# Kernel tuning notes

Measured on AMD Instinct MI355X. Metric: run time of the kernel, lower is better.

The kernel has to match this reference:

```python
import jax, jax.numpy as jnp
import numpy as np

N_NODES = 200_000
N_EDGES = 6_400_000
N_GRAPHS = 512


def _graph_conv(x, src, dst, W_rel, b_rel, W_root, n_nodes):
    # PyG GraphConv (aggr='add'): lin_rel(sum_{j->i} x_j) + lin_root(x_i)
    agg = jax.ops.segment_sum(x[src], dst, num_segments=n_nodes)  # [N, in]
    return agg @ W_rel.T + b_rel + x @ W_root.T


def setup_inputs() -> dict:
    key = jax.random.key(0)
    ks = jax.random.split(key, 12)
    x = jax.random.normal(ks[0], (N_NODES, 3), dtype=jnp.float32)
    edge_index = jax.random.randint(ks[1], (2, N_EDGES), 0, N_NODES, dtype=jnp.int64)
    batch = jnp.sort(jax.random.randint(ks[2], (N_NODES,), 0, N_GRAPHS, dtype=jnp.int64))

    def xavier(k, shape):
        fan_out, fan_in = shape
        lim = np.sqrt(6.0 / (fan_in + fan_out)).astype(np.float32)
        return jax.random.uniform(k, shape, jnp.float32, -lim, lim)

    return {
        "x": x, "edge_index": edge_index, "batch": batch,
        "W1_rel": xavier(ks[3], (32, 3)),  "b1": jnp.zeros((32,), jnp.float32), "W1_root": xavier(ks[4], (32, 3)),
        "W2_rel": xavier(ks[5], (16, 32)), "b2": jnp.zeros((16,), jnp.float32), "W2_root": xavier(ks[6], (16, 32)),
        "W3_rel": xavier(ks[7], (8, 16)),  "b3": jnp.zeros((8,), jnp.float32),  "W3_root": xavier(ks[8], (8, 16)),
        "W_lin": xavier(ks[9], (1, 8)),    "b_lin": jnp.zeros((1,), jnp.float32),
    }


def reference(x, edge_index, batch,
              W1_rel, b1, W1_root,
              W2_rel, b2, W2_root,
              W3_rel, b3, W3_root,
              W_lin, b_lin):
    src, dst = edge_index[0], edge_index[1]
    h = jax.nn.relu(_graph_conv(x, src, dst, W1_rel, b1, W1_root, N_NODES))
    h = jax.nn.relu(_graph_conv(h, src, dst, W2_rel, b2, W2_root, N_NODES))
    h = jax.nn.relu(_graph_conv(h, src, dst, W3_rel, b3, W3_root, N_NODES))
    pooled = jax.ops.segment_max(h, batch, num_segments=N_GRAPHS)  # [G, 8]
    out = pooled @ W_lin.T + b_lin  # [G, 1]
    return out[:, 0]
```

## Files before the change

### kernel.cpp

```cpp
#include <hip/hip_runtime.h>
#include <hip/hip_fp16.h>

#define N_NODES 200000
#define N_EDGES 6400000
#define N_GRAPHS 512
#define HALFN 100000

#define NB1 196
#define CB 1024
#define NSB 16
#define NFB (NB1 * NSB)
#define CHUNK 4096
#define NCH 1563
#define NGRP 25
#define CPG 63
#define SCAP 3072
#define NBLK32 (N_NODES / 32)

typedef float vf4 __attribute__((ext_vector_type(4)));
typedef float vf2 __attribute__((ext_vector_type(2)));
typedef unsigned vu2 __attribute__((ext_vector_type(2)));

__device__ __forceinline__ unsigned ntload_u(const unsigned* p) {
  return __builtin_nontemporal_load(p);
}
__device__ __forceinline__ int ntload_i(const int* p) { return __builtin_nontemporal_load(p); }
__device__ __forceinline__ float ntload_f(const float* p) {
  return __builtin_nontemporal_load(p);
}
__device__ __forceinline__ void ntstore_u(unsigned* p, unsigned v) {
  __builtin_nontemporal_store(v, p);
}

__global__ __launch_bounds__(256) void count_kernel(const int* __restrict__ dst,
                                                    unsigned short* __restrict__ H) {
  __shared__ unsigned hist[4][NB1];
  int t = threadIdx.x, w = t >> 6;
  for (int i = t; i < 4 * NB1; i += 256) ((unsigned*)hist)[i] = 0;
  __syncthreads();
  int c = blockIdx.x;
  long e0 = (long)c * CHUNK;
  long rem = (long)N_EDGES - e0;
  int n = rem > CHUNK ? CHUNK : (int)rem;
  for (int i = t; i < n; i += 256) atomicAdd(&hist[w][dst[e0 + i] >> 10], 1u);
  __syncthreads();
  for (int b = t; b < NB1; b += 256)
    H[(size_t)c * NB1 + b] =
        (unsigned short)(hist[0][b] + hist[1][b] + hist[2][b] + hist[3][b]);
}

__global__ __launch_bounds__(256) void scan_bins1_kernel(unsigned short* __restrict__ H,
                                                         unsigned* __restrict__ P) {
  int b = blockIdx.x * 256 + threadIdx.x;
  int g = blockIdx.y;
  if (b >= NB1) return;
  int c0 = g * CPG, c1 = min(NCH, (g + 1) * CPG);
  unsigned run = 0;
  for (int c = c0; c < c1; c++) {
    unsigned t = H[(size_t)c * NB1 + b];
    H[(size_t)c * NB1 + b] = (unsigned short)run;
    run += t;
  }
  P[(size_t)g * NB1 + b] = run;
}

__global__ __launch_bounds__(256) void scan_bins2_kernel(unsigned* __restrict__ P,
                                                         unsigned* __restrict__ bucketTotal) {
  int b = blockIdx.x * 256 + threadIdx.x;
  if (b >= NB1) return;
  unsigned run = 0;
  for (int g = 0; g < NGRP; g++) {
    unsigned t = P[(size_t)g * NB1 + b];
    P[(size_t)g * NB1 + b] = run;
    run += t;
  }
  bucketTotal[b] = run;
}

__global__ __launch_bounds__(256) void scan_total_kernel(const unsigned* __restrict__ bucketTotal,
                                                         unsigned* __restrict__ bucketStart) {
  __shared__ unsigned partial[256];
  int t = threadIdx.x;
  unsigned v = (t < NB1) ? bucketTotal[t] : 0u;
  partial[t] = v;
  __syncthreads();
  for (int off = 1; off < 256; off <<= 1) {
    unsigned add = (t >= off) ? partial[t - off] : 0u;
    __syncthreads();
    partial[t] += add;
    __syncthreads();
  }
  if (t < NB1) bucketStart[t] = partial[t] - v;
  if (t == 0) bucketStart[NB1] = N_EDGES;
}

__global__ __launch_bounds__(256) void scatterA_kernel(
    const int* __restrict__ src, const int* __restrict__ dst,
    const unsigned short* __restrict__ H, const unsigned* __restrict__ P,
    const unsigned* __restrict__ bucketStart, unsigned* __restrict__ X1) {
  __shared__ unsigned ssort[CHUNK];
  __shared__ unsigned char sbort[CHUNK];
  __shared__ unsigned histw[4][NB1];
  __shared__ unsigned curw[4][NB1];
  __shared__ unsigned gbase[NB1];
  __shared__ unsigned partial[256];
  int t = threadIdx.x, w = t >> 6;
  int c = blockIdx.x;
  int g = c / CPG;
  long e0 = (long)c * CHUNK;
  long rem = (long)N_EDGES - e0;
  int n = rem > CHUNK ? CHUNK : (int)rem;
  for (int i = t; i < 4 * NB1; i += 256) ((unsigned*)histw)[i] = 0;
  __syncthreads();
  for (int i = t; i < n; i += 256) atomicAdd(&histw[w][dst[e0 + i] >> 10], 1u);
  __syncthreads();
  unsigned tot = 0, h0 = 0, h1 = 0, h2 = 0, h3 = 0;
  if (t < NB1) {
    h0 = histw[0][t]; h1 = histw[1][t]; h2 = histw[2][t]; h3 = histw[3][t];
    tot = h0 + h1 + h2 + h3;
  }
  partial[t] = tot;
  __syncthreads();
  for (int off = 1; off < 256; off <<= 1) {
    unsigned add = (t >= off) ? partial[t - off] : 0u;
    __syncthreads();
    partial[t] += add;
    __syncthreads();
  }
  if (t < NB1) {
    unsigned ex = partial[t] - tot;
    unsigned r = ex;
    curw[0][t] = r; r += h0;
    curw[1][t] = r; r += h1;
    curw[2][t] = r; r += h2;
    curw[3][t] = r;
    gbase[t] = bucketStart[t] + P[(size_t)g * NB1 + t] + (unsigned)H[(size_t)c * NB1 + t] - ex;
  }
  __syncthreads();
  for (int i = t; i < n; i += 256) {
    int d = dst[e0 + i], s = src[e0 + i];
    int b = d >> 10;
    unsigned r = atomicAdd(&curw[w][b], 1u);
    ssort[r] = ((unsigned)s << 10) | (unsigned)(d & 1023);
    sbort[r] = (unsigned char)b;
  }
  __syncthreads();
  for (int j = t; j < n; j += 256) X1[gbase[sbort[j]] + j] = ssort[j];
}

__global__ __launch_bounds__(1024) void scatterB_kernel(
    const unsigned* __restrict__ X1, const unsigned* __restrict__ bucketStart,
    unsigned* __restrict__ X2, unsigned* __restrict__ fineStart) {
  __shared__ unsigned histw[16][NSB];
  __shared__ unsigned binstart[NSB + 1];
  __shared__ unsigned cur[NSB];
  int t = threadIdx.x, w = t >> 6, b = blockIdx.x;
  unsigned cs0 = bucketStart[b], cs1 = bucketStart[b + 1];
  int n = (int)(cs1 - cs0);
  if (t < 16 * NSB) ((unsigned*)histw)[t] = 0;
  __syncthreads();
  for (int i = t; i < n; i += 1024)
    atomicAdd(&histw[w][(X1[cs0 + i] >> 6) & 15u], 1u);
  __syncthreads();
  if (t == 0) {
    unsigned run = 0;
    for (int k = 0; k < NSB; k++) {
      binstart[k] = run;
      unsigned tot = 0;
      for (int ww = 0; ww < 16; ww++) tot += histw[ww][k];
      run += tot;
    }
    binstart[NSB] = run;
  }
  __syncthreads();
  if (t < NSB) {
    fineStart[b * NSB + t] = cs0 + binstart[t];
    cur[t] = binstart[t];
  }
  if (b == NB1 - 1 && t == 0) fineStart[NFB] = cs1;
  __syncthreads();
  for (int i = t; i < n; i += 1024) {
    unsigned v = X1[cs0 + i];
    unsigned pos = atomicAdd(&cur[(v >> 6) & 15u], 1u);
    X2[cs0 + pos] = v;
  }
}

__global__ __launch_bounds__(256) void sort2_kernel(const unsigned* __restrict__ X2,
                                                    const unsigned* __restrict__ fineStart,
                                                    unsigned* __restrict__ packedB,
                                                    unsigned* __restrict__ nodeStart,
                                                    unsigned char* __restrict__ deltaSplit) {
  __shared__ unsigned buf[SCAP];
  __shared__ unsigned buf2[SCAP];
  __shared__ unsigned hist[128], base[128], cur[128];
  int t = threadIdx.x, b = blockIdx.x;
  unsigned s0 = fineStart[b], s1 = fineStart[b + 1];
  int n = (int)(s1 - s0);
  if (t < 128) hist[t] = 0;
  for (int i = t; i < n; i += 256) buf[i] = ntload_u(&X2[s0 + i]);
  __syncthreads();
  for (int i = t; i < n; i += 256) {
    unsigned v = buf[i];
    unsigned bin = ((v & 63u) << 1) | ((v >> 10) >= HALFN ? 1u : 0u);
    atomicAdd(&hist[bin], 1u);
  }
  __syncthreads();
  if (t == 0) {
    unsigned run = 0;
    for (int k = 0; k < 128; k++) {
      unsigned v = hist[k];
      base[k] = run;
      cur[k] = run;
      run += v;
    }
  }
  __syncthreads();
  if (t < 64) {
    int gn = b * 64 + t;
    if (gn <= N_NODES) nodeStart[gn] = s0 + base[2 * t];
    if (gn < N_NODES) deltaSplit[gn] = (unsigned char)(base[2 * t + 1] - base[2 * t]);
  }
  for (int i = t; i < n; i += 256) {
    unsigned v = buf[i];
    unsigned bin = ((v & 63u) << 1) | ((v >> 10) >= HALFN ? 1u : 0u);
    unsigned pos = atomicAdd(&cur[bin], 1u);
    buf2[pos] = v >> 10;
  }
  __syncthreads();
  for (int i = t; i < n; i += 256) ntstore_u(&packedB[s0 + i], buf2[i]);
}

__global__ __launch_bounds__(256) void xpad_kernel(const float* __restrict__ x,
                                                   float4* __restrict__ xp) {
  int n = blockIdx.x * 256 + threadIdx.x;
  if (n >= N_NODES) return;
  xp[n] = make_float4(x[3 * n], x[3 * n + 1], x[3 * n + 2], 0.f);
}

__device__ __forceinline__ void half8_unpack(uint4 g, float* f) {
  const __half2* h2 = reinterpret_cast<const __half2*>(&g);
#pragma unroll
  for (int j = 0; j < 4; j++) {
    float2 fj = __half22float2(h2[j]);
    f[2 * j] = fj.x;
    f[2 * j + 1] = fj.y;
  }
}

__global__ __launch_bounds__(256) void layer1a_kernel(
    const unsigned* __restrict__ packed, const unsigned* __restrict__ nodeStart,
    const float4* __restrict__ xp, float* __restrict__ agg) {
  __shared__ float plds[256 * 9];
  int t = threadIdx.x, ln = t >> 3, p = t & 7;
  int node = blockIdx.x * 32 + ln;
  unsigned s1v = ntload_u(&nodeStart[node + 1]);
  float a0 = 0.f, a1 = 0.f, a2 = 0.f;
  for (unsigned base = ntload_u(&nodeStart[node]) + p; base < s1v; base += 32) {
    unsigned i1 = base + 8, i2 = base + 16, i3 = base + 24;
    unsigned e0 = ntload_u(&packed[base]);
    unsigned e1 = ntload_u(&packed[i1]);
    unsigned e2 = ntload_u(&packed[i2]);
    unsigned e3 = ntload_u(&packed[i3]);
    float4 g0 = xp[e0], g1 = xp[e1], g2 = xp[e2], g3 = xp[e3];
    float m1 = (i1 < s1v) ? 1.f : 0.f;
    float m2 = (i2 < s1v) ? 1.f : 0.f;
    float m3 = (i3 < s1v) ? 1.f : 0.f;
    a0 += g0.x + m1 * g1.x + m2 * g2.x + m3 * g3.x;
    a1 += g0.y + m1 * g1.y + m2 * g2.y + m3 * g3.y;
    a2 += g0.z + m1 * g1.z + m2 * g2.z + m3 * g3.z;
  }
  plds[t * 9] = a0; plds[t * 9 + 1] = a1; plds[t * 9 + 2] = a2;
  __syncthreads();
  if (p < 4) {
    int q0 = ln * 72 + p;
    float v = 0.f;
    if (p < 3)
      v = plds[q0] + plds[q0 + 9] + plds[q0 + 18] + plds[q0 + 27] +
          plds[q0 + 36] + plds[q0 + 45] + plds[q0 + 54] + plds[q0 + 63];
    agg[(size_t)node * 4 + p] = v;
  }
}

__global__ __launch_bounds__(256) void layer1b_kernel(
    const float4* __restrict__ xp, const float4* __restrict__ agg,
    const float* __restrict__ W1_rel, const float* __restrict__ b1,
    const float* __restrict__ W1_root,
    const float* __restrict__ W2_rel, const float* __restrict__ W2_root,
    uint4* __restrict__ t2h4, float4* __restrict__ r24) {
  __shared__ float sW1rel[96], sW1root[96], sb1[32], sW2rel[512], sW2root[512];
  for (int i = threadIdx.x; i < 96; i += 256) { sW1rel[i] = W1_rel[i]; sW1root[i] = W1_root[i]; }
  for (int i = threadIdx.x; i < 32; i += 256) sb1[i] = b1[i];
  for (int i = threadIdx.x; i < 512; i += 256) { sW2rel[i] = W2_rel[i]; sW2root[i] = W2_root[i]; }
  __syncthreads();
  int node = blockIdx.x * 256 + threadIdx.x;
  if (node >= N_NODES) return;
  float4 A = agg[node];
  float4 xv = xp[node];
  float h[32];
#pragma unroll
  for (int k = 0; k < 32; k++) {
    float v = sW1rel[3 * k] * A.x + sW1rel[3 * k + 1] * A.y + sW1rel[3 * k + 2] * A.z +
              sW1root[3 * k] * xv.x + sW1root[3 * k + 1] * xv.y + sW1root[3 * k + 2] * xv.z +
              sb1[k];
    h[k] = fmaxf(v, 0.f);
  }
  unsigned tp[8];
#pragma unroll
  for (int j = 0; j < 16; j += 2) {
    float t0 = 0.f, t1 = 0.f;
#pragma unroll
    for (int k = 0; k < 32; k++) {
      t0 += sW2rel[32 * j + k] * h[k];
      t1 += sW2rel[32 * (j + 1) + k] * h[k];
    }
    __half2 pk = __halves2half2(__float2half_rn(t0), __float2half_rn(t1));
    tp[j >> 1] = *(unsigned*)&pk;
  }
  t2h4[(size_t)node * 2] = make_uint4(tp[0], tp[1], tp[2], tp[3]);
  t2h4[(size_t)node * 2 + 1] = make_uint4(tp[4], tp[5], tp[6], tp[7]);
#pragma unroll
  for (int q = 0; q < 4; q++) {
    float rv[4];
#pragma unroll
    for (int jj = 0; jj < 4; jj++) {
      int j = 4 * q + jj;
      float a = 0.f;
#pragma unroll
      for (int k = 0; k < 32; k++) a += sW2root[32 * j + k] * h[k];
      rv[jj] = a;
    }
    r24[(size_t)node * 4 + q] = make_float4(rv[0], rv[1], rv[2], rv[3]);
  }
}

__global__ __launch_bounds__(256) void layer2g_kernel(
    const unsigned* __restrict__ packed, const unsigned* __restrict__ nodeStart,
    const unsigned char* __restrict__ deltaSplit,
    const uint4* __restrict__ t2h4, __half* __restrict__ agg2, int pass) {
  __shared__ float plds[256 * 17];
  int t = threadIdx.x, ln = t >> 3, p = t & 7;
  int node = blockIdx.x * 32 + ln;
  unsigned s0n = ntload_u(&nodeStart[node]);
  unsigned s1n = ntload_u(&nodeStart[node + 1]);
  unsigned split = s0n + (unsigned)deltaSplit[node];
  unsigned lo = pass ? split : s0n;
  unsigned hi = pass ? s1n : split;
  float acc[16];
#pragma unroll
  for (int j = 0; j < 16; j++) acc[j] = 0.f;
  for (unsigned base = lo + p; base < hi; base += 16) {
    unsigned i1 = base + 8;
    unsigned e0 = ntload_u(&packed[base]);
    unsigned e1r = ntload_u(&packed[i1]);
    bool in1 = i1 < hi;
    unsigned e1 = in1 ? e1r : e0;
    uint4 g0a = t2h4[(size_t)e0 * 2], g0b = t2h4[(size_t)e0 * 2 + 1];
    uint4 g1a = t2h4[(size_t)e1 * 2], g1b = t2h4[(size_t)e1 * 2 + 1];
    float f0[16], f1[16];
    half8_unpack(g0a, f0);
    half8_unpack(g0b, f0 + 8);
    half8_unpack(g1a, f1);
    half8_unpack(g1b, f1 + 8);
    float m1 = in1 ? 1.f : 0.f;
#pragma unroll
    for (int j = 0; j < 16; j++) acc[j] += f0[j] + m1 * f1[j];
  }
#pragma unroll
  for (int j = 0; j < 16; j++) plds[t * 17 + j] = acc[j];
  __syncthreads();
  int qb = ln * 8 * 17;
  float s0 = 0.f, s1 = 0.f;
#pragma unroll
  for (int k = 0; k < 8; k++) {
    s0 += plds[qb + k * 17 + 2 * p];
    s1 += plds[qb + k * 17 + 2 * p + 1];
  }
  __half* dst = &agg2[(size_t)node * 16 + 2 * p];
  if (pass) {
    __half2 old = *(const __half2*)dst;
    float2 of = __half22float2(old);
    s0 += of.x;
    s1 += of.y;
  }
  *(__half2*)dst = __halves2half2(__float2half_rn(s0), __float2half_rn(s1));
}

__global__ __launch_bounds__(256) void layer2e_kernel(
    const uint4* agg2q, const float4* __restrict__ r24,
    const float* __restrict__ b2, const float* __restrict__ W3_rel,
    const float* __restrict__ W3_root, uint4* __restrict__ t3h4, float4* r34) {
  __shared__ float sW3rel[128], sW3root[128], sb2[16];
  for (int i = threadIdx.x; i < 128; i += 256) { sW3rel[i] = W3_rel[i]; sW3root[i] = W3_root[i]; }
  if (threadIdx.x < 16) sb2[threadIdx.x] = b2[threadIdx.x];
  __syncthreads();
  int node = blockIdx.x * 256 + threadIdx.x;
  if (node >= N_NODES) return;
  uint4 ga = agg2q[(size_t)node * 2];
  uint4 gb = agg2q[(size_t)node * 2 + 1];
  float ag[16];
  half8_unpack(ga, ag);
  half8_unpack(gb, ag + 8);
  float h[16];
#pragma unroll
  for (int q = 0; q < 4; q++) {
    float4 rv = r24[(size_t)node * 4 + q];
    h[4 * q] = fmaxf(ag[4 * q] + rv.x + sb2[4 * q], 0.f);
    h[4 * q + 1] = fmaxf(ag[4 * q + 1] + rv.y + sb2[4 * q + 1], 0.f);
    h[4 * q + 2] = fmaxf(ag[4 * q + 2] + rv.z + sb2[4 * q + 2], 0.f);
    h[4 * q + 3] = fmaxf(ag[4 * q + 3] + rv.w + sb2[4 * q + 3], 0.f);
  }
  unsigned tp[4];
#pragma unroll
  for (int j = 0; j < 8; j += 2) {
    float t0 = 0.f, t1 = 0.f;
#pragma unroll
    for (int k = 0; k < 16; k++) {
      t0 += sW3rel[16 * j + k] * h[k];
      t1 += sW3rel[16 * (j + 1) + k] * h[k];
    }
    __half2 pk = __halves2half2(__float2half_rn(t0), __float2half_rn(t1));
    tp[j >> 1] = *(unsigned*)&pk;
  }
  t3h4[node] = make_uint4(tp[0], tp[1], tp[2], tp[3]);
  float rv[8];
#pragma unroll
  for (int j = 0; j < 8; j++) {
    float a = 0.f;
#pragma unroll
    for (int k = 0; k < 16; k++) a += sW3root[16 * j + k] * h[k];
    rv[j] = a;
  }
  r34[(size_t)node * 2] = make_float4(rv[0], rv[1], rv[2], rv[3]);
  r34[(size_t)node * 2 + 1] = make_float4(rv[4], rv[5], rv[6], rv[7]);
}

__global__ __launch_bounds__(256) void layer3_kernel(
    const unsigned* __restrict__ packed, const unsigned* __restrict__ nodeStart,
    const uint4* __restrict__ t3h4, const float* __restrict__ r3,
    const float* __restrict__ b3,
    const int* __restrict__ batch, unsigned* __restrict__ pooled) {
  __shared__ float plds[256 * 9];
  __shared__ float sb3[8];
  __shared__ int sgid[32];
  if (threadIdx.x < 8) sb3[threadIdx.x] = b3[threadIdx.x];
  __syncthreads();
  int t = threadIdx.x, ln = t >> 3, p = t & 7;
  int node = blockIdx.x * 32 + ln;
  unsigned s1v = ntload_u(&nodeStart[node + 1]);
  float acc[8];
#pragma unroll
  for (int j = 0; j < 8; j++) acc[j] = 0.f;
  for (unsigned base = ntload_u(&nodeStart[node]) + p; base < s1v; base += 32) {
    unsigned i1 = base + 8, i2 = base + 16, i3 = base + 24;
    unsigned e0 = ntload_u(&packed[base]);
    unsigned e1 = ntload_u(&packed[i1]);
    unsigned e2 = ntload_u(&packed[i2]);
    unsigned e3 = ntload_u(&packed[i3]);
    uint4 g0 = t3h4[e0];
    uint4 g1 = t3h4[e1];
    uint4 g2 = t3h4[e2];
    uint4 g3 = t3h4[e3];
    float m1 = (i1 < s1v) ? 1.f : 0.f;
    float m2 = (i2 < s1v) ? 1.f : 0.f;
    float m3 = (i3 < s1v) ? 1.f : 0.f;
    float f0[8], f1[8], f2[8], f3[8];
    half8_unpack(g0, f0);
    half8_unpack(g1, f1);
    half8_unpack(g2, f2);
    half8_unpack(g3, f3);
#pragma unroll
    for (int j = 0; j < 8; j++)
      acc[j] += f0[j] + m1 * f1[j] + m2 * f2[j] + m3 * f3[j];
  }
#pragma unroll
  for (int j = 0; j < 8; j++) plds[t * 9 + j] = acc[j];
  __syncthreads();
  int gg = ntload_i(&batch[node]);
  int q0 = ln * 72 + p;
  float v = plds[q0] + plds[q0 + 9] + plds[q0 + 18] + plds[q0 + 27] +
            plds[q0 + 36] + plds[q0 + 45] + plds[q0 + 54] + plds[q0 + 63];
  float h = fmaxf(v + sb3[p] + ntload_f(&r3[(size_t)node * 8 + p]), 0.f);
  __syncthreads();
  plds[ln * 9 + p] = h;
  if (p == 0) sgid[ln] = gg;
  __syncthreads();
  if (t < 8) {
    int gcur = sgid[0];
    float m = plds[t];
    for (int l = 1; l < 32; l++) {
      int g2 = sgid[l];
      float hv = plds[l * 9 + t];
      if (g2 != gcur) {
        atomicMax(&pooled[8 * gcur + t], __float_as_uint(m));
        gcur = g2;
        m = hv;
      } else {
        m = fmaxf(m, hv);
      }
    }
    atomicMax(&pooled[8 * gcur + t], __float_as_uint(m));
  }
}

__global__ __launch_bounds__(256) void final_kernel(
    const unsigned* __restrict__ pooled, const float* __restrict__ W_lin,
    const float* __restrict__ b_lin, float* __restrict__ out) {
  int g = blockIdx.x * blockDim.x + threadIdx.x;
  if (g >= N_GRAPHS) return;
  float acc = b_lin[0];
#pragma unroll
  for (int f = 0; f < 8; f++) acc += __uint_as_float(pooled[8 * g + f]) * W_lin[f];
  out[g] = acc;
}

extern "C" void kernel_launch(void* const* d_in, const int* in_sizes, int n_in,
                              void* d_out, int out_size, void* d_ws, size_t ws_size,
                              hipStream_t stream) {
  const float* x = (const float*)d_in[0];
  const int* ei = (const int*)d_in[1];
  const int* src = ei;
  const int* dst = ei + N_EDGES;
  const int* batch = (const int*)d_in[2];
  const float* W1_rel = (const float*)d_in[3];
  const float* b1 = (const float*)d_in[4];
  const float* W1_root = (const float*)d_in[5];
  const float* W2_rel = (const float*)d_in[6];
  const float* b2 = (const float*)d_in[7];
  const float* W2_root = (const float*)d_in[8];
  const float* W3_rel = (const float*)d_in[9];
  const float* b3 = (const float*)d_in[10];
  const float* W3_root = (const float*)d_in[11];
  const float* W_lin = (const float*)d_in[12];
  const float* b_lin = (const float*)d_in[13];
  float* out = (float*)d_out;

  char* ws = (char*)d_ws;
  unsigned* X2 = (unsigned*)(ws + 0);
  float* r2 = (float*)(ws + 0);
  float* agg = (float*)(ws + 12800000);
  __half* agg2 = (__half*)(ws + 12800000);
  float* r3 = (float*)(ws + 12800000);
  unsigned* t3h = (unsigned*)(ws + 19200000);
  float4* xpad = (float4*)(ws + 22400000);
  unsigned* X1 = (unsigned*)(ws + 25600000);
  unsigned* packedB = (unsigned*)(ws + 25600000);
  unsigned* t2h = (unsigned*)(ws + 51200128);
  unsigned short* H = (unsigned short*)(ws + 51200128);
  unsigned* P = (unsigned*)(ws + 51812824);
  unsigned* bucketTotal = (unsigned*)(ws + 51832424);
  unsigned* bucketStart = (unsigned*)(ws + 51833208);
  unsigned* fineStart = (unsigned*)(ws + 51833996);
  unsigned* pooled = (unsigned*)(ws + 57600128);
  unsigned char* deltaSplit = (unsigned char*)(ws + 57616512);
  unsigned* nodeStart = (unsigned*)(ws + 57954016);

  hipMemsetAsync(pooled, 0, N_GRAPHS * 8 * sizeof(unsigned), stream);
  hipMemsetAsync(packedB + N_EDGES, 0, 128, stream);

  count_kernel<<<NCH, 256, 0, stream>>>(dst, H);
  scan_bins1_kernel<<<dim3((NB1 + 255) / 256, NGRP), 256, 0, stream>>>(H, P);
  scan_bins2_kernel<<<(NB1 + 255) / 256, 256, 0, stream>>>(P, bucketTotal);
  scan_total_kernel<<<1, 256, 0, stream>>>(bucketTotal, bucketStart);
  scatterA_kernel<<<NCH, 256, 0, stream>>>(src, dst, H, P, bucketStart, X1);
  scatterB_kernel<<<NB1, 1024, 0, stream>>>(X1, bucketStart, X2, fineStart);
  sort2_kernel<<<NFB, 256, 0, stream>>>(X2, fineStart, packedB, nodeStart, deltaSplit);
  xpad_kernel<<<(N_NODES + 255) / 256, 256, 0, stream>>>(x, xpad);

  layer1a_kernel<<<NBLK32, 256, 0, stream>>>(packedB, nodeStart, xpad, agg);
  layer1b_kernel<<<(N_NODES + 255) / 256, 256, 0, stream>>>(
      xpad, (const float4*)agg, W1_rel, b1, W1_root, W2_rel, W2_root,
      (uint4*)t2h, (float4*)r2);

  layer2g_kernel<<<NBLK32, 256, 0, stream>>>(packedB, nodeStart, deltaSplit,
                                             (const uint4*)t2h, agg2, 0);
  layer2g_kernel<<<NBLK32, 256, 0, stream>>>(packedB, nodeStart, deltaSplit,
                                             (const uint4*)t2h, agg2, 1);
  layer2e_kernel<<<(N_NODES + 255) / 256, 256, 0, stream>>>(
      (const uint4*)agg2, (const float4*)r2, b2, W3_rel, W3_root,
      (uint4*)t3h, (float4*)r3);

  layer3_kernel<<<NBLK32, 256, 0, stream>>>(packedB, nodeStart, (const uint4*)t3h, r3, b3,
                                            batch, pooled);
  final_kernel<<<(N_GRAPHS + 255) / 256, 256, 0, stream>>>(pooled, W_lin, b_lin, out);
}
```

Measured before the change: 425.0 us.

## Fuse layer-1 aggregation into sort2 via shared-memory atomics, store r2 in half

The layer-1 neighbour sum is computed inside the sort2 kernel, which already has each node-group's edges in shared memory. It gathers fp16-packed x and accumulates into per-node shared atomics, so the separate layer1a pass over the CSR is removed. The x padding now emits half precision and runs before the sort, and the layer-2 root term r2 is stored as fp16 instead of fp32 to halve its traffic. In exchange, sort2 does extra random gathers and shared float atomics, and fp16 inputs and r2 lose precision.

```diff
diff --git a/kernel.cpp b/kernel.cpp
--- a/kernel.cpp
+++ b/kernel.cpp
@@ -186,24 +186,71 @@
   }
 }
 
+__global__ __launch_bounds__(256) void xpad_kernel(const float* __restrict__ x,
+                                                   uint2* __restrict__ xph) {
+  int n = blockIdx.x * 256 + threadIdx.x;
+  if (n >= N_NODES) return;
+  __half2 a = __floats2half2_rn(x[3 * n], x[3 * n + 1]);
+  __half2 b = __floats2half2_rn(x[3 * n + 2], 0.f);
+  xph[n] = make_uint2(*(unsigned*)&a, *(unsigned*)&b);
+}
+
 __global__ __launch_bounds__(256) void sort2_kernel(const unsigned* __restrict__ X2,
                                                     const unsigned* __restrict__ fineStart,
+                                                    const uint2* __restrict__ xph,
                                                     unsigned* __restrict__ packedB,
                                                     unsigned* __restrict__ nodeStart,
-                                                    unsigned char* __restrict__ deltaSplit) {
+                                                    unsigned char* __restrict__ deltaSplit,
+                                                    float* __restrict__ agg) {
   __shared__ unsigned buf[SCAP];
   __shared__ unsigned buf2[SCAP];
   __shared__ unsigned hist[128], base[128], cur[128];
+  __shared__ float sacc[256];
   int t = threadIdx.x, b = blockIdx.x;
   unsigned s0 = fineStart[b], s1 = fineStart[b + 1];
   int n = (int)(s1 - s0);
   if (t < 128) hist[t] = 0;
+  sacc[t] = 0.f;
   for (int i = t; i < n; i += 256) buf[i] = ntload_u(&X2[s0 + i]);
   __syncthreads();
-  for (int i = t; i < n; i += 256) {
-    unsigned v = buf[i];
-    unsigned bin = ((v & 63u) << 1) | ((v >> 10) >= HALFN ? 1u : 0u);
-    atomicAdd(&hist[bin], 1u);
+  for (int i0 = t; i0 < n; i0 += 1024) {
+    int i1 = i0 + 256, i2 = i0 + 512, i3 = i0 + 768;
+    unsigned v0 = buf[i0];
+    unsigned v1 = (i1 < n) ? buf[i1] : v0;
+    unsigned v2 = (i2 < n) ? buf[i2] : v0;
+    unsigned v3 = (i3 < n) ? buf[i3] : v0;
+    uint2 g0 = xph[v0 >> 10];
+    uint2 g1 = xph[v1 >> 10];
+    uint2 g2 = xph[v2 >> 10];
+    uint2 g3 = xph[v3 >> 10];
+    atomicAdd(&hist[((v0 & 63u) << 1) | ((v0 >> 10) >= HALFN ? 1u : 0u)], 1u);
+    if (i1 < n) atomicAdd(&hist[((v1 & 63u) << 1) | ((v1 >> 10) >= HALFN ? 1u : 0u)], 1u);
+    if (i2 < n) atomicAdd(&hist[((v2 & 63u) << 1) | ((v2 >> 10) >= HALFN ? 1u : 0u)], 1u);
+    if (i3 < n) atomicAdd(&hist[((v3 & 63u) << 1) | ((v3 >> 10) >= HALFN ? 1u : 0u)], 1u);
+    {
+      float2 xy = __half22float2(*(const __half2*)&g0.x);
+      float2 zw = __half22float2(*(const __half2*)&g0.y);
+      int nd = (v0 & 63u) * 4;
+      atomicAdd(&sacc[nd], xy.x); atomicAdd(&sacc[nd + 1], xy.y); atomicAdd(&sacc[nd + 2], zw.x);
+    }
+    if (i1 < n) {
+      float2 xy = __half22float2(*(const __half2*)&g1.x);
+      float2 zw = __half22float2(*(const __half2*)&g1.y);
+      int nd = (v1 & 63u) * 4;
+      atomicAdd(&sacc[nd], xy.x); atomicAdd(&sacc[nd + 1], xy.y); atomicAdd(&sacc[nd + 2], zw.x);
+    }
+    if (i2 < n) {
+      float2 xy = __half22float2(*(const __half2*)&g2.x);
+      float2 zw = __half22float2(*(const __half2*)&g2.y);
+      int nd = (v2 & 63u) * 4;
+      atomicAdd(&sacc[nd], xy.x); atomicAdd(&sacc[nd + 1], xy.y); atomicAdd(&sacc[nd + 2], zw.x);
+    }
+    if (i3 < n) {
+      float2 xy = __half22float2(*(const __half2*)&g3.x);
+      float2 zw = __half22float2(*(const __half2*)&g3.y);
+      int nd = (v3 & 63u) * 4;
+      atomicAdd(&sacc[nd], xy.x); atomicAdd(&sacc[nd + 1], xy.y); atomicAdd(&sacc[nd + 2], zw.x);
+    }
   }
   __syncthreads();
   if (t == 0) {
@@ -221,6 +268,10 @@
     if (gn <= N_NODES) nodeStart[gn] = s0 + base[2 * t];
     if (gn < N_NODES) deltaSplit[gn] = (unsigned char)(base[2 * t + 1] - base[2 * t]);
   }
+  {
+    int gn = b * 64 + (t >> 2);
+    if (gn < N_NODES) agg[(size_t)gn * 4 + (t & 3)] = sacc[t];
+  }
   for (int i = t; i < n; i += 256) {
     unsigned v = buf[i];
     unsigned bin = ((v & 63u) << 1) | ((v >> 10) >= HALFN ? 1u : 0u);
@@ -231,13 +282,6 @@
   for (int i = t; i < n; i += 256) ntstore_u(&packedB[s0 + i], buf2[i]);
 }
 
-__global__ __launch_bounds__(256) void xpad_kernel(const float* __restrict__ x,
-                                                   float4* __restrict__ xp) {
-  int n = blockIdx.x * 256 + threadIdx.x;
-  if (n >= N_NODES) return;
-  xp[n] = make_float4(x[3 * n], x[3 * n + 1], x[3 * n + 2], 0.f);
-}
-
 __device__ __forceinline__ void half8_unpack(uint4 g, float* f) {
   const __half2* h2 = reinterpret_cast<const __half2*>(&g);
 #pragma unroll
@@ -248,46 +292,12 @@
   }
 }
 
-__global__ __launch_bounds__(256) void layer1a_kernel(
-    const unsigned* __restrict__ packed, const unsigned* __restrict__ nodeStart,
-    const float4* __restrict__ xp, float* __restrict__ agg) {
-  __shared__ float plds[256 * 9];
-  int t = threadIdx.x, ln = t >> 3, p = t & 7;
-  int node = blockIdx.x * 32 + ln;
-  unsigned s1v = ntload_u(&nodeStart[node + 1]);
-  float a0 = 0.f, a1 = 0.f, a2 = 0.f;
-  for (unsigned base = ntload_u(&nodeStart[node]) + p; base < s1v; base += 32) {
-    unsigned i1 = base + 8, i2 = base + 16, i3 = base + 24;
-    unsigned e0 = ntload_u(&packed[base]);
-    unsigned e1 = ntload_u(&packed[i1]);
-    unsigned e2 = ntload_u(&packed[i2]);
-    unsigned e3 = ntload_u(&packed[i3]);
-    float4 g0 = xp[e0], g1 = xp[e1], g2 = xp[e2], g3 = xp[e3];
-    float m1 = (i1 < s1v) ? 1.f : 0.f;
-    float m2 = (i2 < s1v) ? 1.f : 0.f;
-    float m3 = (i3 < s1v) ? 1.f : 0.f;
-    a0 += g0.x + m1 * g1.x + m2 * g2.x + m3 * g3.x;
-    a1 += g0.y + m1 * g1.y + m2 * g2.y + m3 * g3.y;
-    a2 += g0.z + m1 * g1.z + m2 * g2.z + m3 * g3.z;
-  }
-  plds[t * 9] = a0; plds[t * 9 + 1] = a1; plds[t * 9 + 2] = a2;
-  __syncthreads();
-  if (p < 4) {
-    int q0 = ln * 72 + p;
-    float v = 0.f;
-    if (p < 3)
-      v = plds[q0] + plds[q0 + 9] + plds[q0 + 18] + plds[q0 + 27] +
-          plds[q0 + 36] + plds[q0 + 45] + plds[q0 + 54] + plds[q0 + 63];
-    agg[(size_t)node * 4 + p] = v;
-  }
-}
-
 __global__ __launch_bounds__(256) void layer1b_kernel(
-    const float4* __restrict__ xp, const float4* __restrict__ agg,
+    const float* __restrict__ x, const float4* __restrict__ agg,
     const float* __restrict__ W1_rel, const float* __restrict__ b1,
     const float* __restrict__ W1_root,
     const float* __restrict__ W2_rel, const float* __restrict__ W2_root,
-    uint4* __restrict__ t2h4, float4* __restrict__ r24) {
+    uint4* __restrict__ t2h4, uint4* __restrict__ r2h4) {
   __shared__ float sW1rel[96], sW1root[96], sb1[32], sW2rel[512], sW2root[512];
   for (int i = threadIdx.x; i < 96; i += 256) { sW1rel[i] = W1_rel[i]; sW1root[i] = W1_root[i]; }
   for (int i = threadIdx.x; i < 32; i += 256) sb1[i] = b1[i];
@@ -296,12 +306,12 @@
   int node = blockIdx.x * 256 + threadIdx.x;
   if (node >= N_NODES) return;
   float4 A = agg[node];
-  float4 xv = xp[node];
+  float xv0 = x[3 * node], xv1 = x[3 * node + 1], xv2 = x[3 * node + 2];
   float h[32];
 #pragma unroll
   for (int k = 0; k < 32; k++) {
     float v = sW1rel[3 * k] * A.x + sW1rel[3 * k + 1] * A.y + sW1rel[3 * k + 2] * A.z +
-              sW1root[3 * k] * xv.x + sW1root[3 * k + 1] * xv.y + sW1root[3 * k + 2] * xv.z +
+              sW1root[3 * k] * xv0 + sW1root[3 * k + 1] * xv1 + sW1root[3 * k + 2] * xv2 +
               sb1[k];
     h[k] = fmaxf(v, 0.f);
   }
@@ -319,19 +329,20 @@
   }
   t2h4[(size_t)node * 2] = make_uint4(tp[0], tp[1], tp[2], tp[3]);
   t2h4[(size_t)node * 2 + 1] = make_uint4(tp[4], tp[5], tp[6], tp[7]);
-#pragma unroll
-  for (int q = 0; q < 4; q++) {
-    float rv[4];
-#pragma unroll
-    for (int jj = 0; jj < 4; jj++) {
-      int j = 4 * q + jj;
-      float a = 0.f;
-#pragma unroll
-      for (int k = 0; k < 32; k++) a += sW2root[32 * j + k] * h[k];
-      rv[jj] = a;
-    }
-    r24[(size_t)node * 4 + q] = make_float4(rv[0], rv[1], rv[2], rv[3]);
-  }
+  unsigned rp[8];
+#pragma unroll
+  for (int j = 0; j < 16; j += 2) {
+    float r0 = 0.f, r1 = 0.f;
+#pragma unroll
+    for (int k = 0; k < 32; k++) {
+      r0 += sW2root[32 * j + k] * h[k];
+      r1 += sW2root[32 * (j + 1) + k] * h[k];
+    }
+    __half2 pk = __halves2half2(__float2half_rn(r0), __float2half_rn(r1));
+    rp[j >> 1] = *(unsigned*)&pk;
+  }
+  r2h4[(size_t)node * 2] = make_uint4(rp[0], rp[1], rp[2], rp[3]);
+  r2h4[(size_t)node * 2 + 1] = make_uint4(rp[4], rp[5], rp[6], rp[7]);
 }
 
 __global__ __launch_bounds__(256) void layer2g_kernel(
@@ -387,7 +398,7 @@
 }
 
 __global__ __launch_bounds__(256) void layer2e_kernel(
-    const uint4* agg2q, const float4* __restrict__ r24,
+    const uint4* agg2q, const uint4* __restrict__ r2h4,
     const float* __restrict__ b2, const float* __restrict__ W3_rel,
     const float* __restrict__ W3_root, uint4* __restrict__ t3h4, float4* r34) {
   __shared__ float sW3rel[128], sW3root[128], sb2[16];
@@ -401,15 +412,14 @@
   float ag[16];
   half8_unpack(ga, ag);
   half8_unpack(gb, ag + 8);
+  uint4 ra = r2h4[(size_t)node * 2];
+  uint4 rb = r2h4[(size_t)node * 2 + 1];
+  float rv2[16];
+  half8_unpack(ra, rv2);
+  half8_unpack(rb, rv2 + 8);
   float h[16];
 #pragma unroll
-  for (int q = 0; q < 4; q++) {
-    float4 rv = r24[(size_t)node * 4 + q];
-    h[4 * q] = fmaxf(ag[4 * q] + rv.x + sb2[4 * q], 0.f);
-    h[4 * q + 1] = fmaxf(ag[4 * q + 1] + rv.y + sb2[4 * q + 1], 0.f);
-    h[4 * q + 2] = fmaxf(ag[4 * q + 2] + rv.z + sb2[4 * q + 2], 0.f);
-    h[4 * q + 3] = fmaxf(ag[4 * q + 3] + rv.w + sb2[4 * q + 3], 0.f);
-  }
+  for (int k = 0; k < 16; k++) h[k] = fmaxf(ag[k] + rv2[k] + sb2[k], 0.f);
   unsigned tp[4];
 #pragma unroll
   for (int j = 0; j < 8; j += 2) {
@@ -537,26 +547,28 @@
 
   char* ws = (char*)d_ws;
   unsigned* X2 = (unsigned*)(ws + 0);
-  float* r2 = (float*)(ws + 0);
-  float* agg = (float*)(ws + 12800000);
-  __half* agg2 = (__half*)(ws + 12800000);
-  float* r3 = (float*)(ws + 12800000);
-  unsigned* t3h = (unsigned*)(ws + 19200000);
-  float4* xpad = (float4*)(ws + 22400000);
+  uint4* r2h = (uint4*)(ws + 0);
+  __half* agg2 = (__half*)(ws + 6400000);
+  float* r3 = (float*)(ws + 6400000);
+  unsigned* t3h = (unsigned*)(ws + 12800000);
+  unsigned* t2h = (unsigned*)(ws + 16000000);
   unsigned* X1 = (unsigned*)(ws + 25600000);
   unsigned* packedB = (unsigned*)(ws + 25600000);
-  unsigned* t2h = (unsigned*)(ws + 51200128);
   unsigned short* H = (unsigned short*)(ws + 51200128);
   unsigned* P = (unsigned*)(ws + 51812824);
   unsigned* bucketTotal = (unsigned*)(ws + 51832424);
   unsigned* bucketStart = (unsigned*)(ws + 51833208);
   unsigned* fineStart = (unsigned*)(ws + 51833996);
+  float* agg = (float*)(ws + 52000000);
+  uint2* xpadh = (uint2*)(ws + 55300000);
   unsigned* pooled = (unsigned*)(ws + 57600128);
   unsigned char* deltaSplit = (unsigned char*)(ws + 57616512);
   unsigned* nodeStart = (unsigned*)(ws + 57954016);
 
   hipMemsetAsync(pooled, 0, N_GRAPHS * 8 * sizeof(unsigned), stream);
   hipMemsetAsync(packedB + N_EDGES, 0, 128, stream);
+
+  xpad_kernel<<<(N_NODES + 255) / 256, 256, 0, stream>>>(x, xpadh);
 
   count_kernel<<<NCH, 256, 0, stream>>>(dst, H);
   scan_bins1_kernel<<<dim3((NB1 + 255) / 256, NGRP), 256, 0, stream>>>(H, P);
@@ -564,20 +576,19 @@
   scan_total_kernel<<<1, 256, 0, stream>>>(bucketTotal, bucketStart);
   scatterA_kernel<<<NCH, 256, 0, stream>>>(src, dst, H, P, bucketStart, X1);
   scatterB_kernel<<<NB1, 1024, 0, stream>>>(X1, bucketStart, X2, fineStart);
-  sort2_kernel<<<NFB, 256, 0, stream>>>(X2, fineStart, packedB, nodeStart, deltaSplit);
-  xpad_kernel<<<(N_NODES + 255) / 256, 256, 0, stream>>>(x, xpad);
-
-  layer1a_kernel<<<NBLK32, 256, 0, stream>>>(packedB, nodeStart, xpad, agg);
+  sort2_kernel<<<NFB, 256, 0, stream>>>(X2, fineStart, xpadh, packedB, nodeStart,
+                                        deltaSplit, agg);
+
   layer1b_kernel<<<(N_NODES + 255) / 256, 256, 0, stream>>>(
-      xpad, (const float4*)agg, W1_rel, b1, W1_root, W2_rel, W2_root,
-      (uint4*)t2h, (float4*)r2);
+      x, (const float4*)agg, W1_rel, b1, W1_root, W2_rel, W2_root,
+      (uint4*)t2h, r2h);
 
   layer2g_kernel<<<NBLK32, 256, 0, stream>>>(packedB, nodeStart, deltaSplit,
                                              (const uint4*)t2h, agg2, 0);
   layer2g_kernel<<<NBLK32, 256, 0, stream>>>(packedB, nodeStart, deltaSplit,
                                              (const uint4*)t2h, agg2, 1);
   layer2e_kernel<<<(N_NODES + 255) / 256, 256, 0, stream>>>(
-      (const uint4*)agg2, (const float4*)r2, b2, W3_rel, W3_root,
+      (const uint4*)agg2, (const uint4*)r2h, b2, W3_rel, W3_root,
       (uint4*)t3h, (float4*)r3);
 
   layer3_kernel<<<NBLK32, 256, 0, stream>>>(packedB, nodeStart, (const uint4*)t3h, r3, b3,
```

Measured after the change: 474.3 us. 11.6% more time.
